# Performance work log

Hardware: AMD Instinct MI355X
Metric: run time of the kernel (lower is better)

## Reference

```python
import jax, jax.numpy as jnp
import numpy as np

DIM = 512
B, S = 4, 2048


def _linear_params(key, d_in, d_out):
    kw, kb = jax.random.split(key)
    bound = 1.0 / np.sqrt(d_in)
    W = jax.random.uniform(kw, (d_out, d_in), minval=-bound, maxval=bound, dtype=jnp.float32)
    b = jax.random.uniform(kb, (d_out,), minval=-bound, maxval=bound, dtype=jnp.float32)
    return W, b


def setup_inputs() -> dict:
    key = jax.random.key(0)
    ks = jax.random.split(key, 6)
    x = jax.random.normal(ks[0], (B, S, DIM), dtype=jnp.float32)
    Wq, bq = _linear_params(ks[1], DIM, DIM)
    Wk, bk = _linear_params(ks[2], DIM, DIM)
    Wv, bv = _linear_params(ks[3], DIM, DIM)
    W1, b1 = _linear_params(ks[4], DIM, 4 * DIM)
    W2, b2 = _linear_params(ks[5], 4 * DIM, DIM)
    return {"x": x, "Wq": Wq, "bq": bq, "Wk": Wk, "bk": bk,
            "Wv": Wv, "bv": bv, "W1": W1, "b1": b1, "W2": W2, "b2": b2}


def reference(x, Wq, bq, Wk, bk, Wv, bv, W1, b1, W2, b2):
    # q, k, v projections (torch Linear: x @ W.T + b)
    q = x @ Wq.T + bq          # [B, S, D]
    k = x @ Wk.T + bk
    v = x @ Wv.T + bv
    # unscaled attention, exactly as in the source (no 1/sqrt(d))
    scores = jnp.einsum('bsd,btd->bst', q, k)   # [B, S, S]
    attn = jax.nn.softmax(scores, axis=-1) @ v  # [B, S, D]
    # 2-layer FFN with ReLU
    h = jax.nn.relu(attn @ W1.T + b1)           # [B, S, 4D]
    return h @ W2.T + b2                        # [B, S, D]
```

## Files before the change

kernel.cpp:

```cpp
#include <hip/hip_runtime.h>
#include <hip/hip_bf16.h>

typedef _Float16  f16x8  __attribute__((ext_vector_type(8)));
typedef float     f32x4  __attribute__((ext_vector_type(4)));
typedef unsigned short u16;
typedef u16       u16x4  __attribute__((ext_vector_type(4)));
typedef u16       u16x8  __attribute__((ext_vector_type(8)));

__device__ __forceinline__ u16 f2h_bits(float f) {
    union { _Float16 h; u16 u; } v; v.h = (_Float16)f; return v.u;
}

__global__ __launch_bounds__(256)
void cvt_all(const float* __restrict__ x,
             const float* __restrict__ Wq, const float* __restrict__ Wk,
             const float* __restrict__ Wv, const float* __restrict__ W1,
             const float* __restrict__ W2, const float* __restrict__ bq,
             const float* __restrict__ bk, const float* __restrict__ bv,
             u16* __restrict__ x16, u16* __restrict__ Wqkv16,
             u16* __restrict__ W116, u16* __restrict__ W216, float* __restrict__ bqkv) {
    const int i = blockIdx.x * 256 + threadIdx.x;
    constexpr int X4 = 8192 * 512 / 4;
    constexpr int S = 512 * 512 / 4, L = 2048 * 512 / 4;
    const float* src; u16* dst; int j;
    if      (i < X4)                 { src = x;  dst = x16;            j = i;                  }
    else if (i < X4 + S)             { src = Wq; dst = Wqkv16;         j = i - X4;             }
    else if (i < X4 + 2 * S)         { src = Wk; dst = Wqkv16 + 4 * S; j = i - X4 - S;         }
    else if (i < X4 + 3 * S)         { src = Wv; dst = Wqkv16 + 8 * S; j = i - X4 - 2 * S;     }
    else if (i < X4 + 3 * S + L)     { src = W1; dst = W116;           j = i - X4 - 3 * S;     }
    else if (i < X4 + 3 * S + 2 * L) { src = W2; dst = W216;           j = i - X4 - 3 * S - L; }
    else if (i < X4 + 3 * S + 2 * L + 384) {
        const int g = (i - X4 - 3 * S - 2 * L) * 4;
#pragma unroll
        for (int t = 0; t < 4; ++t) {
            const int e = g + t;
            bqkv[e] = (e < 512) ? bq[e] : (e < 1024 ? bk[e - 512] : bv[e - 1024]);
        }
        return;
    } else return;
    f32x4 v = ((const f32x4*)src)[j];
    u16x4 h;
#pragma unroll
    for (int t = 0; t < 4; ++t) h[t] = f2h_bits(v[t]);
    ((u16x4*)dst)[j] = h;
}

template<int ROWS, int NW>
__device__ __forceinline__ void stage_rows(const u16* __restrict__ g0, int ld, u16* lds, int wl) {
    const int l = threadIdx.x & 63;
    constexpr int CH = ROWS / 16 / NW;
#pragma unroll
    for (int i = 0; i < CH; ++i) {
        const int base = (wl * CH + i) << 10;
        const int off  = base + (l << 4);
        const int row  = off >> 6;
        const int cb   = off & 63;
        const u16* g = g0 + (size_t)row * ld + (cb >> 1);
        __builtin_amdgcn_global_load_lds((const __attribute__((address_space(1))) void*)g,
                                         (__attribute__((address_space(3))) void*)((char*)lds + base),
                                         16, 0, 0);
    }
}

template<int BM, int BN, int SPLITK, bool RELU, int OMODE, bool PVS, typename TC>
__global__ __launch_bounds__((BM == 64 ? 128 : 256) * SPLITK, 4)
void gemm16(const u16* __restrict__ Ag, const u16* __restrict__ Bg,
            const float* __restrict__ bias, TC* __restrict__ C,
            void* __restrict__ xtra, const void* __restrict__ xtra2,
            int K, int lda, int ldb, int ldc,
            long sA, long sB, long sC)
{
    const int nx = gridDim.x, ny = gridDim.y;
    const int nwg = nx * ny * gridDim.z;
    int bid = blockIdx.x + nx * (blockIdx.y + ny * blockIdx.z);
    int swz = (bid & 7) * (nwg >> 3) + (bid >> 3);
    const int n0 = (swz % nx) * BN; swz /= nx;
    const int m0 = (swz % ny) * BM;
    const int bz = swz / ny;

    constexpr int WPK = (BM == 64) ? 2 : 4;
    constexpr int FR = (BN == 128) ? 4 : 2;
    constexpr int ATILE = BM * 32;
    constexpr int BTILE = BN * 32;
    constexpr int BUFSZ = ATILE + BTILE;
    __shared__ __align__(16) u16 smem[SPLITK * 2 * BUFSZ];

    const int l  = threadIdx.x & 63, w = threadIdx.x >> 6;
    const int kw = (SPLITK == 2) ? (w / WPK) : 0;
    const int wl = w % WPK;
    const int wr = (BN == 128) ? (wl >> 1) * 64 : wl * 32;
    const int wc = (BN == 128) ? (wl & 1) * 64 : 0;
    const int lr = l & 15, kg = l >> 4;

    const int Kh = K / SPLITK;
    const int kb = kw * Kh;

    const u16* Ab = Ag + (size_t)bz * sA + (size_t)m0 * lda + kb;
    const u16* Bb = Bg + (size_t)bz * sB + (size_t)n0 * ldb + kb;
    const float* Cb = PVS ? ((const float*)xtra2 + (size_t)bz * 32 * 2048) : nullptr;
    C += (size_t)bz * sC;

    u16* mybuf = smem + kw * 2 * BUFSZ;

    auto stage = [&](int buf, int k0) {
        u16* s = mybuf + buf * BUFSZ;
        stage_rows<BM, WPK>(Ab + k0, lda, s, wl);
        stage_rows<BN, WPK>(Bb + k0, ldb, s + ATILE, wl);
    };

    f32x4 acc[FR][4] = {};
    f32x4 tmp[FR][4] = {};
    f32x4 cfp[FR];
    auto compute = [&](int buf) {
        const u16* sA = mybuf + buf * BUFSZ;
        const u16* sB = sA + ATILE;
        f16x8 a[FR], b[4];
#pragma unroll
        for (int i = 0; i < FR; ++i) a[i] = *(const f16x8*)&sA[(wr + i * 16 + lr) * 32 + kg * 8];
#pragma unroll
        for (int i = 0; i < 4; ++i)  b[i] = *(const f16x8*)&sB[(wc + i * 16 + lr) * 32 + kg * 8];
#pragma unroll
        for (int mi = 0; mi < FR; ++mi)
#pragma unroll
            for (int ni = 0; ni < 4; ++ni) {
                if constexpr (PVS)
                    tmp[mi][ni] = __builtin_amdgcn_mfma_f32_16x16x32_f16(a[mi], b[ni], tmp[mi][ni], 0, 0, 0);
                else
                    acc[mi][ni] = __builtin_amdgcn_mfma_f32_16x16x32_f16(a[mi], b[ni], acc[mi][ni], 0, 0, 0);
            }
    };

    stage(0, 0);
    __syncthreads();
    int cur = 0;
    for (int k0 = 0; k0 < Kh; k0 += 32) {
        if (k0 + 32 < Kh) stage(cur ^ 1, k0 + 32);
        if constexpr (PVS) {
            if ((k0 & 32) == 0) {
                const int cb = (kb + k0) >> 6;
#pragma unroll
                for (int mi = 0; mi < FR; ++mi)
                    cfp[mi] = *(const f32x4*)&Cb[(size_t)cb * 2048 + (m0 + wr + mi * 16 + kg * 4)];
            }
        }
        compute(cur);
        if constexpr (PVS) {
            if (k0 & 32) {
#pragma unroll
                for (int mi = 0; mi < FR; ++mi)
#pragma unroll
                    for (int ni = 0; ni < 4; ++ni) {
#pragma unroll
                        for (int j = 0; j < 4; ++j) acc[mi][ni][j] += cfp[mi][j] * tmp[mi][ni][j];
                        tmp[mi][ni] = f32x4{0.f, 0.f, 0.f, 0.f};
                    }
            }
        }
        __syncthreads();
        cur ^= 1;
    }

    if constexpr (SPLITK == 2) {
        float* red = (float*)smem;
        const int slot = (wl * 64 + l) * (FR * 4);
        if (kw == 1) {
#pragma unroll
            for (int mi = 0; mi < FR; ++mi)
#pragma unroll
                for (int ni = 0; ni < 4; ++ni)
                    *(f32x4*)&red[(slot + mi * 4 + ni) * 4] = acc[mi][ni];
        }
        __syncthreads();
        if (kw == 1) return;
#pragma unroll
        for (int mi = 0; mi < FR; ++mi)
#pragma unroll
            for (int ni = 0; ni < 4; ++ni)
                acc[mi][ni] += *(const f32x4*)&red[(slot + mi * 4 + ni) * 4];
    }

    if constexpr (OMODE == 5) {
        float* MB = (float*)xtra + (size_t)bz * 2048 * 32;
        float* SB = (float*)const_cast<void*>(xtra2);
        SB += (size_t)bz * 2048 * 32;
        const int cb = (n0 + wc) >> 6;
#pragma unroll
        for (int mi = 0; mi < FR; ++mi) {
            const int mbase = m0 + wr + mi * 16 + kg * 4;
#pragma unroll
            for (int j = 0; j < 4; ++j) {
                float rmax = fmaxf(fmaxf(acc[mi][0][j], acc[mi][1][j]),
                                   fmaxf(acc[mi][2][j], acc[mi][3][j]));
                rmax = fmaxf(rmax, __shfl_xor(rmax, 1));
                rmax = fmaxf(rmax, __shfl_xor(rmax, 2));
                rmax = fmaxf(rmax, __shfl_xor(rmax, 4));
                rmax = fmaxf(rmax, __shfl_xor(rmax, 8));
                float p[4]; float lsum = 0.0f;
#pragma unroll
                for (int ni = 0; ni < 4; ++ni) { p[ni] = __expf(acc[mi][ni][j] - rmax); lsum += p[ni]; }
                lsum += __shfl_xor(lsum, 1);
                lsum += __shfl_xor(lsum, 2);
                lsum += __shfl_xor(lsum, 4);
                lsum += __shfl_xor(lsum, 8);
                const int row = mbase + j;
                if (lr == 0) {
                    MB[(size_t)row * 32 + cb] = rmax;
                    SB[(size_t)row * 32 + cb] = lsum;
                }
#pragma unroll
                for (int ni = 0; ni < 4; ++ni)
                    ((u16*)C)[(size_t)row * ldc + (n0 + wc + ni * 16 + lr)] = f2h_bits(p[ni]);
            }
        }
        return;
    }

#pragma unroll
    for (int mi = 0; mi < FR; ++mi) {
        const int mbase = m0 + wr + mi * 16 + kg * 4;
#pragma unroll
        for (int ni = 0; ni < 4; ++ni) {
            const int n = n0 + wc + ni * 16 + lr;
            const float bv = bias ? bias[n] : 0.0f;
            if constexpr (OMODE == 4) {
                if (n0 < 1024) {
#pragma unroll
                    for (int j = 0; j < 4; ++j)
                        ((u16*)C)[(size_t)(mbase + j) * ldc + n] = f2h_bits(acc[mi][ni][j] + bv);
                } else {
                    const int d  = n - 1024;
                    const int bb = mbase >> 11;
                    const int s  = mbase & 2047;
                    u16x4 o;
#pragma unroll
                    for (int j = 0; j < 4; ++j) o[j] = f2h_bits(acc[mi][ni][j] + bv);
                    *(u16x4*)((u16*)xtra + ((size_t)bb * 512 + d) * 2048 + s) = o;
                }
            } else {
#pragma unroll
                for (int j = 0; j < 4; ++j) {
                    float x = acc[mi][ni][j] + bv;
                    if constexpr (RELU) x = fmaxf(x, 0.0f);
                    const size_t idx = (size_t)(mbase + j) * ldc + n;
                    if constexpr (OMODE == 0) C[idx] = x;
                    else                      ((u16*)C)[idx] = f2h_bits(x);
                }
            }
        }
    }
}

__global__ __launch_bounds__(256)
void softmax_stats(const float* __restrict__ MB, const float* __restrict__ SB,
                   float* __restrict__ Cf) {
    const int row = blockIdx.x * 256 + threadIdx.x;
    const f32x4* mbp = (const f32x4*)(MB + (size_t)row * 32);
    const f32x4* sbp = (const f32x4*)(SB + (size_t)row * 32);
    f32x4 mv[8], sv[8];
#pragma unroll
    for (int i = 0; i < 8; ++i) { mv[i] = mbp[i]; sv[i] = sbp[i]; }
    float m = mv[0][0];
#pragma unroll
    for (int i = 0; i < 8; ++i)
#pragma unroll
        for (int j = 0; j < 4; ++j) m = fmaxf(m, mv[i][j]);
    float e[8][4]; float s = 0.0f;
#pragma unroll
    for (int i = 0; i < 8; ++i)
#pragma unroll
        for (int j = 0; j < 4; ++j) { e[i][j] = __expf(mv[i][j] - m); s += sv[i][j] * e[i][j]; }
    const float inv = 1.0f / s;
    const int bz = row >> 11, sr = row & 2047;
    float* cp = Cf + (size_t)bz * 32 * 2048 + sr;
#pragma unroll
    for (int i = 0; i < 8; ++i)
#pragma unroll
        for (int j = 0; j < 4; ++j) cp[(size_t)(i * 4 + j) * 2048] = e[i][j] * inv;
}

extern "C" void kernel_launch(void* const* d_in, const int* in_sizes, int n_in,
                              void* d_out, int out_size, void* d_ws, size_t ws_size,
                              hipStream_t stream) {
    const float* x  = (const float*)d_in[0];
    const float* Wq = (const float*)d_in[1];
    const float* bq = (const float*)d_in[2];
    const float* Wk = (const float*)d_in[3];
    const float* bk = (const float*)d_in[4];
    const float* Wv = (const float*)d_in[5];
    const float* bv = (const float*)d_in[6];
    const float* W1 = (const float*)d_in[7];
    const float* b1 = (const float*)d_in[8];
    const float* W2 = (const float*)d_in[9];
    const float* b2 = (const float*)d_in[10];
    float* out = (float*)d_out;

    char* ws = (char*)d_ws;
    size_t off = 0;
    auto alloc = [&](size_t bytes) { void* p = ws + off; off += (bytes + 255) & ~(size_t)255; return p; };
    u16* x16    = (u16*)alloc(8192ull * 512 * 2);
    u16* Wqkv16 = (u16*)alloc(1536ull * 512 * 2);
    u16* W116   = (u16*)alloc(2048ull * 512 * 2);
    u16* W216   = (u16*)alloc(512ull * 2048 * 2);
    float* bqkv = (float*)alloc(1536 * 4);
    u16* qk     = (u16*)alloc(8192ull * 1024 * 2);
    u16* p16    = (u16*)alloc(4ull * 2048 * 2048 * 2);
    u16* vt     = (u16*)alloc(4ull * 512 * 2048 * 2);
    float* mb   = (float*)alloc(8192ull * 32 * 4);
    float* sb   = (float*)alloc(8192ull * 32 * 4);
    float* cf   = (float*)alloc(8192ull * 32 * 4);
    u16* attn = x16;
    u16* h    = p16;
    if (ws_size < off) return;

    dim3 blk(256), blk2(512);

    cvt_all<<<dim3(6914), blk, 0, stream>>>(x, Wq, Wk, Wv, W1, W2, bq, bk, bv,
                                            x16, Wqkv16, W116, W216, bqkv);

    gemm16<128, 128, 1, false, 4, false, u16><<<dim3(12, 64, 1), blk, 0, stream>>>(
        x16, Wqkv16, bqkv, qk, vt, nullptr, 512, 512, 512, 1024, 0, 0, 0);
    gemm16<128, 128, 1, false, 5, false, u16><<<dim3(16, 16, 4), blk, 0, stream>>>(
        qk, qk + 512, nullptr, p16, mb, sb, 512, 1024, 1024, 2048,
        2048L * 1024, 2048L * 1024, 2048L * 2048);
    softmax_stats<<<dim3(32), blk, 0, stream>>>(mb, sb, cf);
    gemm16<64, 64, 2, false, 2, true, u16><<<dim3(8, 32, 4), blk, 0, stream>>>(
        p16, vt, nullptr, attn, nullptr, cf, 2048, 2048, 2048, 512,
        2048L * 2048, 512L * 2048, 2048L * 512);
    gemm16<128, 128, 1, true, 2, false, u16><<<dim3(16, 64, 1), blk, 0, stream>>>(
        attn, W116, b1, h, nullptr, nullptr, 512, 512, 512, 2048, 0, 0, 0);
    gemm16<64, 64, 2, false, 0, false, float><<<dim3(8, 128, 1), blk, 0, stream>>>(
        h, W216, b2, out, nullptr, nullptr, 2048, 2048, 2048, 512, 0, 0, 0);
}
```

Before: 188.9 us.

## Add triple-buffered LDS pipeline and 128-row tiles for split-K GEMMs

Adds a three-stage LDS pipeline for the GEMM kernel. Loads run two K-steps ahead, guarded by explicit vmcnt waits and a raw s_barrier instead of __syncthreads. The two split-K GEMMs (PV and the FFN down-projection) move from 64x64 tiles with 256 threads to 128x64 tiles with 512 threads, halving their grid. The aim is to hide global-load latency and increase reuse per block, at the cost of more LDS, fewer blocks per CU, and hand-tuned waitcnt values that must match the load count.

```diff
diff --git a/kernel.cpp b/kernel.cpp
--- a/kernel.cpp
+++ b/kernel.cpp
@@ -9,6 +9,16 @@
 
 __device__ __forceinline__ u16 f2h_bits(float f) {
     union { _Float16 h; u16 u; } v; v.h = (_Float16)f; return v.u;
+}
+
+template<int N> __device__ __forceinline__ void vmwait() {
+    if constexpr (N == 0)      asm volatile("s_waitcnt vmcnt(0)" ::: "memory");
+    else if constexpr (N == 3) asm volatile("s_waitcnt vmcnt(3)" ::: "memory");
+    else if constexpr (N == 4) asm volatile("s_waitcnt vmcnt(4)" ::: "memory");
+}
+__device__ __forceinline__ void pipe_barrier() {
+    __builtin_amdgcn_s_barrier();
+    __builtin_amdgcn_sched_barrier(0);
 }
 
 __global__ __launch_bounds__(256)
@@ -62,8 +72,8 @@
     }
 }
 
-template<int BM, int BN, int SPLITK, bool RELU, int OMODE, bool PVS, typename TC>
-__global__ __launch_bounds__((BM == 64 ? 128 : 256) * SPLITK, 4)
+template<int BN, int SPLITK, int PIPE, bool RELU, int OMODE, bool PVS, typename TC>
+__global__ __launch_bounds__(256 * SPLITK, 2 * SPLITK)
 void gemm16(const u16* __restrict__ Ag, const u16* __restrict__ Bg,
             const float* __restrict__ bias, TC* __restrict__ C,
             void* __restrict__ xtra, const void* __restrict__ xtra2,
@@ -75,44 +85,45 @@
     int bid = blockIdx.x + nx * (blockIdx.y + ny * blockIdx.z);
     int swz = (bid & 7) * (nwg >> 3) + (bid >> 3);
     const int n0 = (swz % nx) * BN; swz /= nx;
-    const int m0 = (swz % ny) * BM;
+    const int m0 = (swz % ny) * 128;
     const int bz = swz / ny;
 
-    constexpr int WPK = (BM == 64) ? 2 : 4;
     constexpr int FR = (BN == 128) ? 4 : 2;
-    constexpr int ATILE = BM * 32;
+    constexpr int ATILE = 128 * 32;
     constexpr int BTILE = BN * 32;
     constexpr int BUFSZ = ATILE + BTILE;
-    __shared__ __align__(16) u16 smem[SPLITK * 2 * BUFSZ];
+    constexpr int LPT = 2 + BN / 64;
+    __shared__ __align__(16) u16 smem[SPLITK * PIPE * BUFSZ];
 
     const int l  = threadIdx.x & 63, w = threadIdx.x >> 6;
-    const int kw = (SPLITK == 2) ? (w / WPK) : 0;
-    const int wl = w % WPK;
+    const int kw = (SPLITK == 2) ? (w >> 2) : 0;
+    const int wl = w & 3;
     const int wr = (BN == 128) ? (wl >> 1) * 64 : wl * 32;
     const int wc = (BN == 128) ? (wl & 1) * 64 : 0;
     const int lr = l & 15, kg = l >> 4;
 
     const int Kh = K / SPLITK;
     const int kb = kw * Kh;
+    const int T  = Kh >> 5;
 
     const u16* Ab = Ag + (size_t)bz * sA + (size_t)m0 * lda + kb;
     const u16* Bb = Bg + (size_t)bz * sB + (size_t)n0 * ldb + kb;
     const float* Cb = PVS ? ((const float*)xtra2 + (size_t)bz * 32 * 2048) : nullptr;
     C += (size_t)bz * sC;
 
-    u16* mybuf = smem + kw * 2 * BUFSZ;
-
-    auto stage = [&](int buf, int k0) {
-        u16* s = mybuf + buf * BUFSZ;
-        stage_rows<BM, WPK>(Ab + k0, lda, s, wl);
-        stage_rows<BN, WPK>(Bb + k0, ldb, s + ATILE, wl);
+    u16* mybuf = smem + kw * PIPE * BUFSZ;
+
+    auto stage = [&](int slot, int t) {
+        u16* s = mybuf + slot * BUFSZ;
+        stage_rows<128, 4>(Ab + t * 32, lda, s, wl);
+        stage_rows<BN, 4>(Bb + t * 32, ldb, s + ATILE, wl);
     };
 
     f32x4 acc[FR][4] = {};
     f32x4 tmp[FR][4] = {};
     f32x4 cfp[FR];
-    auto compute = [&](int buf) {
-        const u16* sA = mybuf + buf * BUFSZ;
+    auto compute = [&](int slot) {
+        const u16* sA = mybuf + slot * BUFSZ;
         const u16* sB = sA + ATILE;
         f16x8 a[FR], b[4];
 #pragma unroll
@@ -129,23 +140,19 @@
                     acc[mi][ni] = __builtin_amdgcn_mfma_f32_16x16x32_f16(a[mi], b[ni], acc[mi][ni], 0, 0, 0);
             }
     };
-
-    stage(0, 0);
-    __syncthreads();
-    int cur = 0;
-    for (int k0 = 0; k0 < Kh; k0 += 32) {
-        if (k0 + 32 < Kh) stage(cur ^ 1, k0 + 32);
+    auto pvs_pre = [&](int t) {
         if constexpr (PVS) {
-            if ((k0 & 32) == 0) {
-                const int cb = (kb + k0) >> 6;
+            if ((t & 1) == 0) {
+                const int cb = (kb + t * 32) >> 6;
 #pragma unroll
                 for (int mi = 0; mi < FR; ++mi)
                     cfp[mi] = *(const f32x4*)&Cb[(size_t)cb * 2048 + (m0 + wr + mi * 16 + kg * 4)];
             }
         }
-        compute(cur);
+    };
+    auto pvs_post = [&](int t) {
         if constexpr (PVS) {
-            if (k0 & 32) {
+            if (t & 1) {
 #pragma unroll
                 for (int mi = 0; mi < FR; ++mi)
 #pragma unroll
@@ -156,8 +163,34 @@
                     }
             }
         }
+    };
+
+    if constexpr (PIPE == 3) {
+        stage(0, 0);
+        stage(1, 1);
+        vmwait<LPT>();
+        pipe_barrier();
+        for (int t = 0; t < T; ++t) {
+            if (t + 2 < T) stage((t + 2) % 3, t + 2);
+            pvs_pre(t);
+            compute(t % 3);
+            pvs_post(t);
+            if (t + 2 < T) vmwait<LPT>();
+            else           vmwait<0>();
+            pipe_barrier();
+        }
+    } else {
+        stage(0, 0);
         __syncthreads();
-        cur ^= 1;
+        int cur = 0;
+        for (int t = 0; t < T; ++t) {
+            if (t + 1 < T) stage(cur ^ 1, t + 1);
+            pvs_pre(t);
+            compute(cur);
+            pvs_post(t);
+            __syncthreads();
+            cur ^= 1;
+        }
     }
 
     if constexpr (SPLITK == 2) {
@@ -317,17 +350,17 @@
     cvt_all<<<dim3(6914), blk, 0, stream>>>(x, Wq, Wk, Wv, W1, W2, bq, bk, bv,
                                             x16, Wqkv16, W116, W216, bqkv);
 
-    gemm16<128, 128, 1, false, 4, false, u16><<<dim3(12, 64, 1), blk, 0, stream>>>(
+    gemm16<128, 1, 2, false, 4, false, u16><<<dim3(12, 64, 1), blk, 0, stream>>>(
         x16, Wqkv16, bqkv, qk, vt, nullptr, 512, 512, 512, 1024, 0, 0, 0);
-    gemm16<128, 128, 1, false, 5, false, u16><<<dim3(16, 16, 4), blk, 0, stream>>>(
+    gemm16<128, 1, 2, false, 5, false, u16><<<dim3(16, 16, 4), blk, 0, stream>>>(
         qk, qk + 512, nullptr, p16, mb, sb, 512, 1024, 1024, 2048,
         2048L * 1024, 2048L * 1024, 2048L * 2048);
     softmax_stats<<<dim3(32), blk, 0, stream>>>(mb, sb, cf);
-    gemm16<64, 64, 2, false, 2, true, u16><<<dim3(8, 32, 4), blk, 0, stream>>>(
+    gemm16<64, 2, 3, false, 2, true, u16><<<dim3(8, 16, 4), blk2, 0, stream>>>(
         p16, vt, nullptr, attn, nullptr, cf, 2048, 2048, 2048, 512,
         2048L * 2048, 512L * 2048, 2048L * 512);
-    gemm16<128, 128, 1, true, 2, false, u16><<<dim3(16, 64, 1), blk, 0, stream>>>(
+    gemm16<128, 1, 2, true, 2, false, u16><<<dim3(16, 64, 1), blk, 0, stream>>>(
         attn, W116, b1, h, nullptr, nullptr, 512, 512, 512, 2048, 0, 0, 0);
-    gemm16<64, 64, 2, false, 0, false, float><<<dim3(8, 128, 1), blk, 0, stream>>>(
+    gemm16<64, 2, 3, false, 0, false, float><<<dim3(8, 64, 1), blk2, 0, stream>>>(
         h, W216, b2, out, nullptr, nullptr, 2048, 2048, 2048, 512, 0, 0, 0);
 }
```

Measured after the change: 177.2 us. 6.2% less time.
